# Performance work log

Measured on AMD Instinct MI355X. Metric: run time of the kernel, lower is better.

The kernel has to match this reference:

```python
import jax, jax.numpy as jnp
import numpy as np

H, W = 352, 1216
K = 8                 # points_per_pixel (z-buffer depth)
RADIUS_PX = 1.5       # splat radius in pixels
RAD_POW = 2.0         # opts.rad_pow
TAU = 1.0             # opts.tau


def _rasterize(pts):
    # pts: [B,P,3] with xy in NDC [-1,1], z>0.
    # Returns idx [B,H,W,K] int32 (packed point index, -1 = empty),
    # dist2 [B,H,W,K] squared NDC distance to pixel center, and NDC radius r.
    B, P, _ = pts.shape
    r = RADIUS_PX / max(H, W) * 2.0
    hx = int(np.ceil(r * W / 2.0))   # splat half-extent in pixels (x)
    hy = int(np.ceil(r * H / 2.0))   # splat half-extent in pixels (y)
    dy, dx = np.meshgrid(np.arange(-hy, hy + 1), np.arange(-hx, hx + 1), indexing='ij')
    dy = jnp.asarray(dy.ravel()); dx = jnp.asarray(dx.ravel())     # [Wn]
    x, y, z = pts[..., 0], pts[..., 1], pts[..., 2]                # [B,P]
    i0 = jnp.floor((y + 1.0) * 0.5 * H).astype(jnp.int32)
    j0 = jnp.floor((x + 1.0) * 0.5 * W).astype(jnp.int32)
    ii = i0[..., None] + dy                                        # [B,P,Wn]
    jj = j0[..., None] + dx
    xc = (jj + 0.5) * (2.0 / W) - 1.0                              # pixel centers (NDC)
    yc = (ii + 0.5) * (2.0 / H) - 1.0
    d2 = (x[..., None] - xc) ** 2 + (y[..., None] - yc) ** 2
    valid = (ii >= 0) & (ii < H) & (jj >= 0) & (jj < W) & (d2 < r * r) & (z[..., None] > 0)
    NPIX = B * H * W
    pix = jnp.where(valid, (jnp.arange(B)[:, None, None] * H + ii) * W + jj, NPIX)
    pid = jnp.broadcast_to((jnp.arange(B)[:, None] * P + jnp.arange(P)[None, :])[..., None], pix.shape)
    pixf = pix.reshape(-1)
    zf = jnp.broadcast_to(z[..., None], pix.shape).reshape(-1)
    d2f = d2.reshape(-1)
    pidf = pid.reshape(-1)
    # sort candidates by (pixel, z): gives nearest-first z-buffer ordering per pixel
    order = jnp.lexsort((zf, pixf))
    pixs, d2s, pids = pixf[order], d2f[order], pidf[order]
    first = jnp.searchsorted(pixs, pixs, side='left')
    rank = jnp.arange(pixs.shape[0]) - first      # z-rank within each pixel
    keep = (rank < K) & (pixs < NPIX)
    tp = jnp.where(keep, pixs, NPIX)              # sentinel row NPIX collects rejects
    tr = jnp.where(keep, rank, 0)
    idx = jnp.full((NPIX + 1, K), -1, jnp.int32).at[tp, tr].set(
        jnp.where(keep, pids, -1).astype(jnp.int32))
    dist2 = jnp.zeros((NPIX + 1, K), pts.dtype).at[tp, tr].set(
        jnp.where(keep, d2s, jnp.zeros((), pts.dtype)))
    return idx[:NPIX].reshape(B, H, W, K), dist2[:NPIX].reshape(B, H, W, K), r


def _forward(pts3D, src):
    B, C, P = src.shape
    idx, dist2, r = _rasterize(pts3D)
    dist = dist2 / (r ** RAD_POW)
    alphas = (1.0 - jnp.sqrt(jnp.clip(dist, 0.001, 1.0))) ** TAU   # [B,H,W,K]
    feats = src.transpose(0, 2, 1).reshape(B * P, C)               # features_packed [B*P,C]
    acc = jnp.zeros((B, H, W, C), src.dtype)
    for k in range(K):   # fixed small depth-layer loop: weighted_sum compositing
        ik = idx[..., k]
        wk = jnp.where(ik >= 0, alphas[..., k], 0.0)
        acc = acc + wk[..., None] * feats[jnp.clip(ik, 0)]
    return acc.transpose(0, 3, 1, 2)                               # [B,C,H,W]


def setup_inputs():
    key = jax.random.key(0)
    k1, k2, k3 = jax.random.split(key, 3)
    B, P, C = 2, 65536, 64
    xy = jax.random.uniform(k1, (B, P, 2), minval=-1.0, maxval=1.0)
    z = jax.random.uniform(k2, (B, P, 1), minval=0.5, maxval=20.0)
    pts3D = jnp.concatenate([xy, z], axis=-1)
    src = jax.random.normal(k3, (B, C, P), dtype=jnp.float32)
    return {"pts3D": pts3D, "src": src}


def reference(pts3D, src):
    return _forward(pts3D, src)
```

## Files before the change

### kernel.cpp

```cpp
#include <hip/hip_runtime.h>
#include <cstdint>
#include <cstddef>

#define HH 352
#define WW 1216
#define KK 8
#define PP 65536
#define BB 2
#define CC 64

#define RD (1.5 / 1216.0 * 2.0)


typedef float vf4 __attribute__((ext_vector_type(4)));

static __device__ __forceinline__ unsigned int bf16pack_rn(float a, float b) {
    unsigned int ua = __float_as_uint(a), ub = __float_as_uint(b);
    ua = (ua + 0x7FFFu + ((ua >> 16) & 1u)) >> 16;
    ub = (ub + 0x7FFFu + ((ub >> 16) & 1u)) >> 16;
    return (ub << 16) | ua;
}

static __device__ __forceinline__ void scatter_body(const float* __restrict__ pts,
                                                    unsigned int* __restrict__ slots,
                                                    int tid) {
    const int b = tid >> 16;
    const float x = pts[tid * 3 + 0];
    const float y = pts[tid * 3 + 1];
    const float z = pts[tid * 3 + 2];
    if (!(z > 0.f)) return;

    const int i0 = (int)floorf((y + 1.f) * 0.5f * (float)HH);
    if (i0 < 0 || i0 >= HH) return;
    const int j0 = (int)floorf((x + 1.f) * 0.5f * (float)WW);

    const float yc = ((float)i0 + 0.5f) * (2.f / (float)HH) - 1.f;
    const float dyv = y - yc;
    const float dy2 = dyv * dyv;
    const float r2 = (float)(RD * RD);

    unsigned int fb = __float_as_uint(z) >> 13;
    fb = fb < 0x1F800u ? 0x1F800u : fb;
    fb = fb > 0x217FFu ? 0x217FFu : fb;
    const unsigned int key = ((fb - 0x1F800u) << 17) | (unsigned int)tid;

    const unsigned int rowbase = (unsigned int)(b * HH + i0) * WW;

    #pragma unroll
    for (int dx = -1; dx <= 1; ++dx) {
        const int jj = j0 + dx;
        if (jj < 0 || jj >= WW) continue;
        const float xc = ((float)jj + 0.5f) * (2.f / (float)WW) - 1.f;
        const float dxv = x - xc;
        if (!(dxv * dxv + dy2 < r2)) continue;

        unsigned int* s = slots + (size_t)(rowbase + jj) * KK;
        unsigned int cur = key;
        #pragma unroll
        for (int k = 0; k < KK; ++k) {
            unsigned int old = atomicMin(&s[k], cur);
            if (old & 0x80000000u) break;
            cur = old > cur ? old : cur;
        }
    }
}

#define TRANS_BLOCKS (BB * (PP / 64))
#define SCATTER_BLOCKS ((BB * PP) / 256)

__global__ __launch_bounds__(256) void prep_kernel(const float* __restrict__ pts,
                                                   const float* __restrict__ src,
                                                   unsigned int* __restrict__ slots,
                                                   unsigned int* __restrict__ feats) {
    __shared__ float tile[64][65];
    if (blockIdx.x < TRANS_BLOCKS) {
        const int bid = blockIdx.x;
        const int b = bid >> 10;
        const int p0 = (bid & 1023) * 64;
        const float* sb = src + (size_t)b * CC * PP;
        #pragma unroll
        for (int i = 0; i < 16; ++i) {
            const int idx = threadIdx.x + i * 256;
            const int c = idx >> 6;
            const int p = idx & 63;
            tile[p][c] = sb[(size_t)c * PP + (p0 + p)];
        }
        __syncthreads();
        unsigned int* fbp = feats + ((size_t)b * PP + p0) * (CC / 2);
        #pragma unroll
        for (int i = 0; i < 8; ++i) {
            const int idx = threadIdx.x + i * 256;
            const int p = idx >> 5;
            const int cp = idx & 31;
            fbp[(size_t)p * (CC / 2) + cp] = bf16pack_rn(tile[p][2 * cp], tile[p][2 * cp + 1]);
        }
        return;
    }
    scatter_body(pts, slots, (blockIdx.x - TRANS_BLOCKS) * 256 + threadIdx.x);
}

__global__ __launch_bounds__(256) void scatter_kernel(const float* __restrict__ pts,
                                                      unsigned int* __restrict__ slots) {
    scatter_body(pts, slots, blockIdx.x * 256 + threadIdx.x);
}

__global__ __launch_bounds__(256) void composite_kernel(const float* __restrict__ pts,
                                                        const unsigned int* __restrict__ feats,
                                                        const unsigned int* __restrict__ slots,
                                                        float* __restrict__ out) {
    const int HWp = HH * WW;
    const int lane = threadIdx.x & 63;
    const int cg   = threadIdx.x >> 6;
    const int pix = blockIdx.x * 64 + lane;
    const int b  = pix / HWp;
    const int hw = pix - b * HWp;
    const int h = hw / WW;
    const int w = hw - h * WW;

    const uint4* sv = (const uint4*)(slots + (size_t)pix * KK);
    const uint4 sa = sv[0], sb4 = sv[1];
    const unsigned int keys[KK] = {sa.x, sa.y, sa.z, sa.w, sb4.x, sb4.y, sb4.z, sb4.w};

    const float xc = ((float)w + 0.5f) * (2.f / (float)WW) - 1.f;
    const float yc = ((float)h + 0.5f) * (2.f / (float)HH) - 1.f;
    const float invr2 = (float)(1.0 / (RD * RD));

    float acc[16];
    #pragma unroll
    for (int c = 0; c < 16; ++c) acc[c] = 0.f;

    #pragma unroll
    for (int k = 0; k < KK; ++k) {
        const unsigned int key = keys[k];
        if (key & 0x80000000u) break;
        const int pid = (int)(key & 0x1FFFFu);
        const float px = pts[pid * 3 + 0];
        const float py = pts[pid * 3 + 1];
        const float ddx = px - xc;
        const float ddy = py - yc;
        float dist = (ddx * ddx + ddy * ddy) * invr2;
        dist = fminf(fmaxf(dist, 0.001f), 1.0f);
        const float a = 1.f - sqrtf(dist);

        const uint4* f = (const uint4*)(feats + (size_t)pid * (CC / 2) + cg * 8);
        #pragma unroll
        for (int j = 0; j < 2; ++j) {
            const uint4 q = f[j];
            acc[8 * j + 0] += a * __uint_as_float(q.x << 16);
            acc[8 * j + 1] += a * __uint_as_float(q.x & 0xFFFF0000u);
            acc[8 * j + 2] += a * __uint_as_float(q.y << 16);
            acc[8 * j + 3] += a * __uint_as_float(q.y & 0xFFFF0000u);
            acc[8 * j + 4] += a * __uint_as_float(q.z << 16);
            acc[8 * j + 5] += a * __uint_as_float(q.z & 0xFFFF0000u);
            acc[8 * j + 6] += a * __uint_as_float(q.w << 16);
            acc[8 * j + 7] += a * __uint_as_float(q.w & 0xFFFF0000u);
        }
    }

    __shared__ float lds[4][16][68];
    #pragma unroll
    for (int c = 0; c < 16; ++c) lds[cg][c][lane] = acc[c];
    __syncthreads();

    const int q  = lane & 15;
    const int s  = lane >> 4;
    const int hwq = (blockIdx.x * 64 - b * HWp) + 4 * q;
    float* ob = out + ((size_t)b * CC + (size_t)(cg * 16 + s * 4)) * HWp + hwq;
    #pragma unroll
    for (int j = 0; j < 4; ++j) {
        vf4 v = *(const vf4*)&lds[cg][s * 4 + j][4 * q];
        __builtin_nontemporal_store(v, (vf4*)(ob + (size_t)j * HWp));
    }
}

__global__ __launch_bounds__(256) void composite_direct(const float* __restrict__ pts,
                                                        const float* __restrict__ src,
                                                        const unsigned int* __restrict__ slots,
                                                        float* __restrict__ out) {
    const int HWp = HH * WW;
    const int tid = blockIdx.x * blockDim.x + threadIdx.x;
    const int b = tid / HWp;
    const int hw = tid - b * HWp;
    const int h = hw / WW;
    const int w = hw - h * WW;

    const uint4* sv = (const uint4*)(slots + (size_t)tid * KK);
    const uint4 sa = sv[0], sb4 = sv[1];
    const unsigned int keys[KK] = {sa.x, sa.y, sa.z, sa.w, sb4.x, sb4.y, sb4.z, sb4.w};

    const float xc = ((float)w + 0.5f) * (2.f / (float)WW) - 1.f;
    const float yc = ((float)h + 0.5f) * (2.f / (float)HH) - 1.f;
    const float invr2 = (float)(1.0 / (RD * RD));

    float alpha[KK];
    int   pidx[KK];
    int n = 0;
    #pragma unroll
    for (int k = 0; k < KK; ++k) {
        const unsigned int key = keys[k];
        if (key & 0x80000000u) break;
        const int pid = (int)(key & 0x1FFFFu);
        const float px = pts[pid * 3 + 0];
        const float py = pts[pid * 3 + 1];
        const float ddx = px - xc;
        const float ddy = py - yc;
        float dist = (ddx * ddx + ddy * ddy) * invr2;
        dist = fminf(fmaxf(dist, 0.001f), 1.0f);
        alpha[k] = 1.f - sqrtf(dist);
        pidx[k]  = pid & (PP - 1);
        n = k + 1;
    }

    const float* sbp = src + (size_t)b * CC * PP;
    float* ob = out + (size_t)b * CC * HWp + hw;
    for (int c = 0; c < CC; ++c) {
        float acc = 0.f;
        #pragma unroll
        for (int k = 0; k < KK; ++k)
            if (k < n) acc += alpha[k] * sbp[(size_t)c * PP + pidx[k]];
        __builtin_nontemporal_store(acc, ob + (size_t)c * HWp);
    }
}

extern "C" void kernel_launch(void* const* d_in, const int* in_sizes, int n_in,
                              void* d_out, int out_size, void* d_ws, size_t ws_size,
                              hipStream_t stream) {
    const float* pts = (const float*)d_in[0];
    const float* src = (const float*)d_in[1];
    float* out = (float*)d_out;

    const size_t slot_bytes  = (size_t)BB * HH * WW * KK * sizeof(unsigned int);
    const size_t feats_bytes = (size_t)BB * PP * CC * 2;
    const size_t need = slot_bytes + feats_bytes;

    if (ws_size >= need + 256) {
        char* base = (char*)d_ws + ((ws_size - need) & ~(size_t)255);
        unsigned int* feats = (unsigned int*)base;
        unsigned int* slots = (unsigned int*)(base + feats_bytes);

        prep_kernel<<<TRANS_BLOCKS + SCATTER_BLOCKS, 256, 0, stream>>>(pts, src, slots, feats);
        const int comp_blocks = (BB * HH * WW) / 64;
        composite_kernel<<<comp_blocks, 256, 0, stream>>>(pts, feats, slots, out);
    } else {
        unsigned int* slots = (unsigned int*)d_ws;
        scatter_kernel<<<SCATTER_BLOCKS, 256, 0, stream>>>(pts, slots);
        composite_direct<<<(BB * HH * WW) / 256, 256, 0, stream>>>(pts, src, slots, out);
    }
}
```

Baseline: 258.1 us.

## Compute splat alphas once per pixel in LDS and widen composite blocks

The composite kernel now runs 1024-thread blocks covering 256 pixels. One wave group computes each pixel's point ids and alpha weights once and stores them in shared memory, where the four channel-group waves read them. Previously all four channel groups reloaded the slot keys and point positions and recomputed the sqrt alpha themselves. Output transposition through LDS now writes 256-pixel-wide rows, giving longer contiguous stores. The cost is an extra barrier, three quarters of the block idle during the alpha phase, and much larger LDS use per block, which may reduce occupancy.

```diff
diff --git a/kernel.cpp b/kernel.cpp
--- a/kernel.cpp
+++ b/kernel.cpp
@@ -104,44 +104,69 @@
     scatter_body(pts, slots, blockIdx.x * 256 + threadIdx.x);
 }
 
-__global__ __launch_bounds__(256) void composite_kernel(const float* __restrict__ pts,
-                                                        const unsigned int* __restrict__ feats,
-                                                        const unsigned int* __restrict__ slots,
-                                                        float* __restrict__ out) {
+__global__ __launch_bounds__(1024) void composite_kernel(const float* __restrict__ pts,
+                                                         const unsigned int* __restrict__ feats,
+                                                         const unsigned int* __restrict__ slots,
+                                                         float* __restrict__ out) {
+    __shared__ float lds_t[64][260];
+    uint2* lds_al = (uint2*)&lds_t[0][0];
+    int*   lds_n  = (int*)((char*)&lds_t[0][0] + 18432);
+
     const int HWp = HH * WW;
     const int lane = threadIdx.x & 63;
-    const int cg   = threadIdx.x >> 6;
-    const int pix = blockIdx.x * 64 + lane;
-    const int b  = pix / HWp;
-    const int hw = pix - b * HWp;
-    const int h = hw / WW;
-    const int w = hw - h * WW;
-
-    const uint4* sv = (const uint4*)(slots + (size_t)pix * KK);
-    const uint4 sa = sv[0], sb4 = sv[1];
-    const unsigned int keys[KK] = {sa.x, sa.y, sa.z, sa.w, sb4.x, sb4.y, sb4.z, sb4.w};
-
-    const float xc = ((float)w + 0.5f) * (2.f / (float)WW) - 1.f;
-    const float yc = ((float)h + 0.5f) * (2.f / (float)HH) - 1.f;
+    const int wid  = threadIdx.x >> 6;
+    const int g    = wid >> 2;
+    const int cg   = wid & 3;
+
+    const int px0 = blockIdx.x * 256;
+    const int b   = px0 / HWp;
+    const int hw0 = px0 - b * HWp;
+    const int pl  = g * 64 + lane;
+
     const float invr2 = (float)(1.0 / (RD * RD));
 
+    if (cg == 0) {
+        const int hw = hw0 + pl;
+        const int h = hw / WW;
+        const int w = hw - h * WW;
+        const float xc = ((float)w + 0.5f) * (2.f / (float)WW) - 1.f;
+        const float yc = ((float)h + 0.5f) * (2.f / (float)HH) - 1.f;
+
+        const uint4* sv = (const uint4*)(slots + ((size_t)px0 + pl) * KK);
+        const uint4 sa = sv[0], sb4 = sv[1];
+        const unsigned int keys[KK] = {sa.x, sa.y, sa.z, sa.w, sb4.x, sb4.y, sb4.z, sb4.w};
+
+        int n = 0;
+        #pragma unroll
+        for (int k = 0; k < KK; ++k) {
+            const unsigned int key = keys[k];
+            if (key & 0x80000000u) break;
+            const int pid = (int)(key & 0x1FFFFu);
+            const float px = pts[pid * 3 + 0];
+            const float py = pts[pid * 3 + 1];
+            const float ddx = px - xc;
+            const float ddy = py - yc;
+            float dist = (ddx * ddx + ddy * ddy) * invr2;
+            dist = fminf(fmaxf(dist, 0.001f), 1.0f);
+            const float a = 1.f - sqrtf(dist);
+            lds_al[pl * 9 + k] = make_uint2((unsigned int)pid, __float_as_uint(a));
+            n = k + 1;
+        }
+        lds_n[pl] = n;
+    }
+    __syncthreads();
+
     float acc[16];
     #pragma unroll
     for (int c = 0; c < 16; ++c) acc[c] = 0.f;
 
+    const int n = lds_n[pl];
     #pragma unroll
     for (int k = 0; k < KK; ++k) {
-        const unsigned int key = keys[k];
-        if (key & 0x80000000u) break;
-        const int pid = (int)(key & 0x1FFFFu);
-        const float px = pts[pid * 3 + 0];
-        const float py = pts[pid * 3 + 1];
-        const float ddx = px - xc;
-        const float ddy = py - yc;
-        float dist = (ddx * ddx + ddy * ddy) * invr2;
-        dist = fminf(fmaxf(dist, 0.001f), 1.0f);
-        const float a = 1.f - sqrtf(dist);
-
+        if (k >= n) break;
+        const uint2 e = lds_al[pl * 9 + k];
+        const int pid = (int)e.x;
+        const float a = __uint_as_float(e.y);
         const uint4* f = (const uint4*)(feats + (size_t)pid * (CC / 2) + cg * 8);
         #pragma unroll
         for (int j = 0; j < 2; ++j) {
@@ -156,19 +181,16 @@
             acc[8 * j + 7] += a * __uint_as_float(q.w & 0xFFFF0000u);
         }
     }
-
-    __shared__ float lds[4][16][68];
-    #pragma unroll
-    for (int c = 0; c < 16; ++c) lds[cg][c][lane] = acc[c];
     __syncthreads();
 
-    const int q  = lane & 15;
-    const int s  = lane >> 4;
-    const int hwq = (blockIdx.x * 64 - b * HWp) + 4 * q;
-    float* ob = out + ((size_t)b * CC + (size_t)(cg * 16 + s * 4)) * HWp + hwq;
+    #pragma unroll
+    for (int c = 0; c < 16; ++c) lds_t[cg * 16 + c][pl] = acc[c];
+    __syncthreads();
+
+    float* ob = out + ((size_t)b * CC + (size_t)(wid * 4)) * HWp + hw0 + 4 * lane;
     #pragma unroll
     for (int j = 0; j < 4; ++j) {
-        vf4 v = *(const vf4*)&lds[cg][s * 4 + j][4 * q];
+        vf4 v = *(const vf4*)&lds_t[wid * 4 + j][4 * lane];
         __builtin_nontemporal_store(v, (vf4*)(ob + (size_t)j * HWp));
     }
 }
@@ -239,8 +261,8 @@
         unsigned int* slots = (unsigned int*)(base + feats_bytes);
 
         prep_kernel<<<TRANS_BLOCKS + SCATTER_BLOCKS, 256, 0, stream>>>(pts, src, slots, feats);
-        const int comp_blocks = (BB * HH * WW) / 64;
-        composite_kernel<<<comp_blocks, 256, 0, stream>>>(pts, feats, slots, out);
+        const int comp_blocks = (BB * HH * WW) / 256;
+        composite_kernel<<<comp_blocks, 1024, 0, stream>>>(pts, feats, slots, out);
     } else {
         unsigned int* slots = (unsigned int*)d_ws;
         scatter_kernel<<<SCATTER_BLOCKS, 256, 0, stream>>>(pts, slots);
```

Result: no change. 262.4 us (+1.6%).
